# Kernel tuning notes

Measured on AMD Instinct MI355X. Metric: run time of the kernel, lower is better.

Reference implementation:

```python
import jax, jax.numpy as jnp
import numpy as np

T = 65536
OBS_DIM = 64
ACTION_DIM = 16
EMB_DIM = 8  # min(action_dim, 8)
HID = 256
NOBJ = 4
IN_DIM = OBS_DIM + EMB_DIM


def setup_inputs() -> dict:
    key = jax.random.key(0)
    ks = jax.random.split(key, 16)
    g = lambda k, shape, s=0.05: (jax.random.normal(k, shape, dtype=jnp.float32) * s)
    inp = {
        "observations": jax.random.normal(ks[0], (T, OBS_DIM), dtype=jnp.float32),
        "actions": jax.random.randint(ks[1], (T,), 0, ACTION_DIM),
        "emb": g(ks[2], (ACTION_DIM, EMB_DIM)),
        # layer 0 (input_dim -> hidden)
        "Win0": g(ks[3], (HID, IN_DIM)),
        "WB0": g(ks[4], (HID, IN_DIM)),
        "WC0": g(ks[5], (HID, IN_DIM)),
        "Wd0": g(ks[6], (HID, IN_DIM)),
        "Alog0": jax.random.normal(ks[7], (HID,), dtype=jnp.float32),
        # layer 1 (hidden -> hidden)
        "Win1": g(ks[8], (HID, HID)),
        "WB1": g(ks[9], (HID, HID)),
        "WC1": g(ks[10], (HID, HID)),
        "Wd1": g(ks[11], (HID, HID)),
        "Alog1": jax.random.normal(ks[12], (HID,), dtype=jnp.float32),
        # output head
        "Wout": g(ks[13], (NOBJ, HID)),
        "bout": jnp.zeros((NOBJ,), dtype=jnp.float32),
    }
    return inp


def _ssm_layer(x, Win, WB, WC, Wd, Alog):
    """One selective-SSM layer: h_t = exp(delta_t * A) * h_{t-1} + B_t * x_state_t; y = C * h."""
    x_state = x @ Win.T            # [T, H]
    B = x @ WB.T                   # [T, H]
    C = x @ WC.T                   # [T, H]
    delta = jax.nn.sigmoid(x @ Wd.T)  # [T, H]
    A = -jnp.exp(Alog)             # [H]
    A_bar = jnp.exp(delta * A)     # [T, H], decay factors
    Bx = B * x_state               # [T, H], inputs to the recurrence

    def step(h, inputs):
        a, bx = inputs
        h = a * h + bx
        return h, h

    h0 = jnp.zeros((x_state.shape[-1],), dtype=x_state.dtype)
    _, h_seq = jax.lax.scan(step, h0, (A_bar, Bx))
    return C * h_seq


def reference(observations, actions, emb,
              Win0, WB0, WC0, Wd0, Alog0,
              Win1, WB1, WC1, Wd1, Alog1,
              Wout, bout):
    x = jnp.concatenate([observations, emb[actions]], axis=-1)  # [T, IN_DIM]
    x = _ssm_layer(x, Win0, WB0, WC0, Wd0, Alog0)
    x = _ssm_layer(x, Win1, WB1, WC1, Wd1, Alog1)
    out = x @ Wout.T + bout                                     # [T, NOBJ]
    return jax.nn.softplus(out) + 1.0
```

## Files before the change

kernel.cpp:

```cpp
#include <hip/hip_runtime.h>

typedef unsigned short u16;
typedef __attribute__((ext_vector_type(8))) short bf16x8;
typedef __attribute__((ext_vector_type(4))) float f32x4;
typedef __attribute__((ext_vector_type(8))) unsigned short u16x8;

#define T_LEN 65536
#define HID 256
#define K0 96
#define K1 256
#define BM 128
#define BN 128
#define CHUNK 64
#define NCHUNK 1024
#define NSEG 32
#define CPS 32

__device__ __forceinline__ float bf2f(u16 u) {
  unsigned x = ((unsigned)u) << 16; float f; __builtin_memcpy(&f, &x, 4); return f;
}
__device__ __forceinline__ u16 f2bf(float f) {
  unsigned x; __builtin_memcpy(&x, &f, 4);
  x += 0x7FFFu + ((x >> 16) & 1u);
  return (u16)(x >> 16);
}

__device__ __forceinline__ void gl_lds16(const void* g, void* l) {
  __builtin_amdgcn_global_load_lds((const __attribute__((address_space(1))) unsigned int*)g,
                                   (__attribute__((address_space(3))) unsigned int*)l,
                                   16, 0, 0);
}

__global__ __launch_bounds__(256) void build_x0(
    const float* __restrict__ obs, const int* __restrict__ act,
    const float* __restrict__ emb, u16* __restrict__ x0)
{
  const int idx = blockIdx.x * 256 + threadIdx.x;
  const int t = idx / 24, seg = idx - t * 24;
  u16 v0 = 0, v1 = 0, v2 = 0, v3 = 0;
  if (seg < 16) {
    const float4 f = *(const float4*)&obs[(size_t)t * 64 + seg * 4];
    v0 = f2bf(f.x); v1 = f2bf(f.y); v2 = f2bf(f.z); v3 = f2bf(f.w);
  } else if (seg < 18) {
    const int a = act[t];
    const int e0 = (seg - 16) * 4;
    v0 = f2bf(emb[a * 8 + e0 + 0]); v1 = f2bf(emb[a * 8 + e0 + 1]);
    v2 = f2bf(emb[a * 8 + e0 + 2]); v3 = f2bf(emb[a * 8 + e0 + 3]);
  }
  u16* p = &x0[(size_t)t * 96 + seg * 4];
  p[0] = v0; p[1] = v1; p[2] = v2; p[3] = v3;
}

__global__ __launch_bounds__(256) void prep_w(
    const float* __restrict__ Win0, const float* __restrict__ WB0,
    const float* __restrict__ WC0,  const float* __restrict__ Wd0,
    const float* __restrict__ Alog0,
    const float* __restrict__ Win1, const float* __restrict__ WB1,
    const float* __restrict__ WC1,  const float* __restrict__ Wd1,
    const float* __restrict__ Alog1,
    u16* __restrict__ W0v, u16* __restrict__ W1v, float* __restrict__ Aneg)
{
  const int idx = blockIdx.x * 256 + threadIdx.x;
  if (idx < 1024 * K0) {
    const int row = idx / K0, k = idx - row * K0;
    const int h = row >> 2, p = row & 3;
    const float* W = (p == 0) ? Win0 : (p == 1) ? WB0 : (p == 2) ? WC0 : Wd0;
    W0v[idx] = f2bf((k < 72) ? W[h * 72 + k] : 0.f);
  } else if (idx < 1024 * K0 + 1024 * K1) {
    const int j = idx - 1024 * K0;
    const int row = j >> 8, k = j & 255;
    const int h = row >> 2, p = row & 3;
    const float* W = (p == 0) ? Win1 : (p == 1) ? WB1 : (p == 2) ? WC1 : Wd1;
    W1v[j] = f2bf(W[h * 256 + k]);
  } else if (idx < 1024 * K0 + 1024 * K1 + 512) {
    const int j = idx - (1024 * K0 + 1024 * K1);
    Aneg[j] = -__expf((j < 256) ? Alog0[j] : Alog1[j - 256]);
  }
}

template <int KDIM>
__global__ __launch_bounds__(256, 3) void gemm_scan(
    const u16* __restrict__ X, const u16* __restrict__ Wv,
    const float* __restrict__ Aneg,
    u16* __restrict__ hlocb, u16* __restrict__ apfxb, u16* __restrict__ cb,
    float* __restrict__ aprod, float* __restrict__ hlast)
{
  static_assert(KDIM % 32 == 0, "K must be multiple of 32");
  __shared__ u16 sA[BM * 32];
  __shared__ u16 sB[BN * 32];
  __shared__ float sT[64 * 132];
  __shared__ float sAgg[8 * 32 * 2];

  const int tid = threadIdx.x;
  const int l   = tid & 63;
  const int w   = tid >> 6;
  const int n0  = blockIdx.x * BN;
  const int m0  = blockIdx.y * BM;
  const int wm  = (w >> 1) * 64;
  const int wn  = (w & 1) * 64;

  f32x4 acc[4][4];
  const f32x4 zero = {0.f, 0.f, 0.f, 0.f};
#pragma unroll
  for (int mi = 0; mi < 4; ++mi)
#pragma unroll
    for (int ni = 0; ni < 4; ++ni) acc[mi][ni] = zero;

  const int rr = w * 32 + (l >> 2);
  const int kb = (l & 3) * 16;

  for (int ks = 0; ks < KDIM / 32; ++ks) {
    __syncthreads();
#pragma unroll
    for (int i = 0; i < 2; ++i) {
      const char* gA = (const char*)(X + (size_t)(m0 + rr + i * 16) * KDIM + ks * 32) + kb;
      gl_lds16(gA, (char*)sA + w * 2048 + i * 1024);
      const char* gB = (const char*)(Wv + (size_t)(n0 + rr + i * 16) * KDIM + ks * 32) + kb;
      gl_lds16(gB, (char*)sB + w * 2048 + i * 1024);
    }
    __syncthreads();

    bf16x8 af[4], bfr[4];
#pragma unroll
    for (int mi = 0; mi < 4; ++mi)
      af[mi] = *(const bf16x8*)&sA[(wm + mi * 16 + (l & 15)) * 32 + (l >> 4) * 8];
#pragma unroll
    for (int ni = 0; ni < 4; ++ni)
      bfr[ni] = *(const bf16x8*)&sB[(wn + ni * 16 + (l & 15)) * 32 + (l >> 4) * 8];
#pragma unroll
    for (int mi = 0; mi < 4; ++mi)
#pragma unroll
      for (int ni = 0; ni < 4; ++ni)
        acc[mi][ni] = __builtin_amdgcn_mfma_f32_16x16x32_bf16(af[mi], bfr[ni], acc[mi][ni], 0, 0, 0);
  }

  const int q  = tid >> 5;
  const int c  = tid & 31;
  const int ch = (n0 >> 2) + c;
  const float An = Aneg[ch];

  for (int hh = 0; hh < 2; ++hh) {
    __syncthreads();
    if ((w >> 1) == hh) {
#pragma unroll
      for (int mi = 0; mi < 4; ++mi)
#pragma unroll
        for (int ni = 0; ni < 4; ++ni)
#pragma unroll
          for (int v = 0; v < 4; ++v)
            sT[(mi * 16 + (l >> 4) * 4 + v) * 132 + wn + ni * 16 + (l & 15)] = acc[mi][ni][v];
    }
    __syncthreads();

    float Pl[8], Hl[8];
    float ap = 1.f, hl = 0.f;
#pragma unroll
    for (int j = 0; j < 8; ++j) {
      const int tl = q * 8 + j;
      const float pin = sT[tl * 132 + 4 * c + 0];
      const float pB  = sT[tl * 132 + 4 * c + 1];
      const float pC  = sT[tl * 132 + 4 * c + 2];
      const float pd  = sT[tl * 132 + 4 * c + 3];
      const float delta = 1.f / (1.f + __expf(-pd));
      const float a  = __expf(delta * An);
      hl = a * hl + pB * pin;
      ap *= a;
      Pl[j] = ap; Hl[j] = hl;
      cb[(size_t)(m0 + hh * 64 + tl) * HID + ch] = f2bf(pC);
    }
    sAgg[(q * 32 + c) * 2 + 0] = ap;
    sAgg[(q * 32 + c) * 2 + 1] = hl;
    __syncthreads();

    float sap = 1.f, shl = 0.f;
    for (int qq = 0; qq < q; ++qq) {
      const float a_ = sAgg[(qq * 32 + c) * 2 + 0];
      const float h_ = sAgg[(qq * 32 + c) * 2 + 1];
      shl = a_ * shl + h_;
      sap *= a_;
    }
#pragma unroll
    for (int j = 0; j < 8; ++j) {
      const int tl = q * 8 + j;
      const size_t r = (size_t)(m0 + hh * 64 + tl) * HID + ch;
      hlocb[r] = f2bf(Hl[j] + Pl[j] * shl);
      apfxb[r] = f2bf(Pl[j] * sap);
    }
    if (q == 7) {
      const int chunk = blockIdx.y * 2 + hh;
      aprod[(size_t)chunk * HID + ch] = sap * ap;
      hlast[(size_t)chunk * HID + ch] = Hl[7] + Pl[7] * shl;
    }
  }
}

__global__ __launch_bounds__(256) void pass2a(
    const float* __restrict__ aprod, const float* __restrict__ hlast,
    float* __restrict__ clocal, float* __restrict__ apfxc,
    float* __restrict__ segAP, float* __restrict__ segHL)
{
  const int s = blockIdx.x;
  const int h = threadIdx.x;
  float H = 0.f, P = 1.f;
#pragma unroll 4
  for (int j = 0; j < CPS; ++j) {
    const size_t o = (size_t)(s * CPS + j) * HID + h;
    clocal[o] = H; apfxc[o] = P;
    const float a = aprod[o], hh = hlast[o];
    H = a * H + hh;
    P *= a;
  }
  segAP[s * HID + h] = P;
  segHL[s * HID + h] = H;
}

__global__ __launch_bounds__(256) void pass2b(
    const float* __restrict__ segAP, const float* __restrict__ segHL,
    float* __restrict__ segc)
{
  const int h = threadIdx.x;
  float S = 0.f;
#pragma unroll 4
  for (int s = 0; s < NSEG; ++s) {
    segc[s * HID + h] = S;
    S = segAP[s * HID + h] * S + segHL[s * HID + h];
  }
}

__global__ __launch_bounds__(256) void pass2c(
    const float* __restrict__ clocal, const float* __restrict__ apfxc,
    const float* __restrict__ segc, float* __restrict__ carry)
{
  const int ck = blockIdx.x;
  const int h  = threadIdx.x;
  const size_t o = (size_t)ck * HID + h;
  carry[o] = clocal[o] + apfxc[o] * segc[(ck / CPS) * HID + h];
}

__global__ __launch_bounds__(256) void combine(
    const u16* __restrict__ hlocb, const u16* __restrict__ apfxb,
    const u16* __restrict__ cb, const float* __restrict__ carry,
    u16* __restrict__ y)
{
  const size_t v = (size_t)blockIdx.x * 256 + threadIdx.x;
  const int t   = (int)(v >> 5);
  const int ch0 = ((int)v & 31) * 8;
  const u16x8 hl8 = *(const u16x8*)&hlocb[v * 8];
  const u16x8 ap8 = *(const u16x8*)&apfxb[v * 8];
  const u16x8 c8  = *(const u16x8*)&cb[v * 8];
  const float* cr = &carry[(size_t)(t >> 6) * HID + ch0];
  const float4 cr0 = *(const float4*)&cr[0];
  const float4 cr1 = *(const float4*)&cr[4];
  const float crv[8] = {cr0.x, cr0.y, cr0.z, cr0.w, cr1.x, cr1.y, cr1.z, cr1.w};
  u16x8 o;
#pragma unroll
  for (int j = 0; j < 8; ++j)
    o[j] = f2bf(bf2f((u16)c8[j]) * (bf2f((u16)hl8[j]) + bf2f((u16)ap8[j]) * crv[j]));
  *(u16x8*)&y[v * 8] = o;
}

__global__ __launch_bounds__(256) void head(
    const u16* __restrict__ y1, const float* __restrict__ Wout,
    const float* __restrict__ bout, float* __restrict__ out)
{
  __shared__ u16 ly[64 * 264];
  __shared__ float lw[4 * HID];
  __shared__ float lb[4];
  const int tid = threadIdx.x;
  for (int i = tid; i < 4 * HID; i += 256) lw[i] = Wout[i];
  if (tid < 4) lb[tid] = bout[tid];
  const size_t rbase = (size_t)blockIdx.x * 64 * HID;
#pragma unroll
  for (int i = 0; i < 8; ++i) {
    const int lin = i * 256 + tid;
    const int r = lin >> 5, c8 = lin & 31;
    *(u16x8*)&ly[r * 264 + c8 * 8] = *(const u16x8*)&y1[rbase + (size_t)r * HID + c8 * 8];
  }
  __syncthreads();
  const int t = tid >> 2, o = tid & 3;
  float acc = lb[o];
#pragma unroll 8
  for (int h = 0; h < HID; ++h)
    acc += bf2f(ly[t * 264 + h]) * lw[o * HID + h];
  out[((size_t)blockIdx.x * 64 + t) * 4 + o] = logf(1.f + __expf(acc)) + 1.f;
}

extern "C" void kernel_launch(void* const* d_in, const int* in_sizes, int n_in,
                              void* d_out, int out_size, void* d_ws, size_t ws_size,
                              hipStream_t stream)
{
  (void)in_sizes; (void)n_in; (void)out_size; (void)ws_size;
  const float* obs   = (const float*)d_in[0];
  const int*   act   = (const int*)d_in[1];
  const float* emb   = (const float*)d_in[2];
  const float* Win0  = (const float*)d_in[3];
  const float* WB0   = (const float*)d_in[4];
  const float* WC0   = (const float*)d_in[5];
  const float* Wd0   = (const float*)d_in[6];
  const float* Alog0 = (const float*)d_in[7];
  const float* Win1  = (const float*)d_in[8];
  const float* WB1   = (const float*)d_in[9];
  const float* WC1   = (const float*)d_in[10];
  const float* Wd1   = (const float*)d_in[11];
  const float* Alog1 = (const float*)d_in[12];
  const float* Wout  = (const float*)d_in[13];
  const float* bout  = (const float*)d_in[14];
  float* out = (float*)d_out;

  char* ws = (char*)d_ws;
  size_t off = 0;
  auto alloc = [&](size_t bytes) {
    char* p = ws + off;
    off += (bytes + 255) & ~(size_t)255;
    return p;
  };
  u16*   x0    = (u16*)  alloc((size_t)T_LEN * K0 * 2);
  u16*   W0v   = (u16*)  alloc((size_t)1024 * K0 * 2);
  u16*   W1v   = (u16*)  alloc((size_t)1024 * K1 * 2);
  float* Aneg  = (float*)alloc(512 * 4);
  u16*   hlocb = (u16*)  alloc((size_t)T_LEN * HID * 2);
  u16*   apfxb = (u16*)  alloc((size_t)T_LEN * HID * 2);
  u16*   cb    = (u16*)  alloc((size_t)T_LEN * HID * 2);
  u16*   y     = (u16*)  alloc((size_t)T_LEN * HID * 2);
  float* aprod = (float*)alloc((size_t)NCHUNK * HID * 4);
  float* hlast = (float*)alloc((size_t)NCHUNK * HID * 4);
  float* carry = (float*)alloc((size_t)NCHUNK * HID * 4);
  float* clocal= (float*)alloc((size_t)NCHUNK * HID * 4);
  float* apfxc = (float*)alloc((size_t)NCHUNK * HID * 4);
  float* segAP = (float*)alloc((size_t)NSEG * HID * 4);
  float* segHL = (float*)alloc((size_t)NSEG * HID * 4);
  float* segc  = (float*)alloc((size_t)NSEG * HID * 4);

  build_x0<<<T_LEN * 24 / 256, 256, 0, stream>>>(obs, act, emb, x0);
  prep_w<<<(1024 * K0 + 1024 * K1 + 512 + 255) / 256, 256, 0, stream>>>(
      Win0, WB0, WC0, Wd0, Alog0, Win1, WB1, WC1, Wd1, Alog1, W0v, W1v, Aneg);

  gemm_scan<K0><<<dim3(8, T_LEN / BM), 256, 0, stream>>>(x0, W0v, Aneg,
      hlocb, apfxb, cb, aprod, hlast);
  pass2a<<<NSEG, 256, 0, stream>>>(aprod, hlast, clocal, apfxc, segAP, segHL);
  pass2b<<<1, 256, 0, stream>>>(segAP, segHL, segc);
  pass2c<<<NCHUNK, 256, 0, stream>>>(clocal, apfxc, segc, carry);
  combine<<<T_LEN * HID / 8 / 256, 256, 0, stream>>>(hlocb, apfxb, cb, carry, y);

  gemm_scan<K1><<<dim3(8, T_LEN / BM), 256, 0, stream>>>(y, W1v, Aneg + 256,
      hlocb, apfxb, cb, aprod, hlast);
  pass2a<<<NSEG, 256, 0, stream>>>(aprod, hlast, clocal, apfxc, segAP, segHL);
  pass2b<<<1, 256, 0, stream>>>(segAP, segHL, segc);
  pass2c<<<NCHUNK, 256, 0, stream>>>(clocal, apfxc, segc, carry);
  combine<<<T_LEN * HID / 8 / 256, 256, 0, stream>>>(hlocb, apfxb, cb, carry, y);

  head<<<T_LEN / 64, 256, 0, stream>>>(y, Wout, bout, out);
}
```

Before: 294.3 us.

## Premultiply C into packed bf16 pair, fuse carry into combine, XCD-aware tile mapping

The scan kernel now multiplies C into the local state and the prefix product and stores both as one packed 32-bit bf16 pair, instead of three separate bf16 arrays. This cuts intermediate traffic from 6 to 4 bytes per element on both write and read. The pass2c kernel is removed and its carry computation is folded into combine. Blocks are remapped to a 1D grid so each XCD handles a contiguous range of row tiles, which aims to improve L2 locality. Rounding C*h to bf16 before adding the carry term changes numerics slightly.

```diff
diff --git a/kernel.cpp b/kernel.cpp
--- a/kernel.cpp
+++ b/kernel.cpp
@@ -82,7 +82,7 @@
 __global__ __launch_bounds__(256, 3) void gemm_scan(
     const u16* __restrict__ X, const u16* __restrict__ Wv,
     const float* __restrict__ Aneg,
-    u16* __restrict__ hlocb, u16* __restrict__ apfxb, u16* __restrict__ cb,
+    unsigned* __restrict__ uvb,
     float* __restrict__ aprod, float* __restrict__ hlast)
 {
   static_assert(KDIM % 32 == 0, "K must be multiple of 32");
@@ -94,8 +94,13 @@
   const int tid = threadIdx.x;
   const int l   = tid & 63;
   const int w   = tid >> 6;
-  const int n0  = blockIdx.x * BN;
-  const int m0  = blockIdx.y * BM;
+  const int bid = blockIdx.x;
+  const int xcd = bid & 7;
+  const int k_  = bid >> 3;
+  const int mt  = xcd * 64 + (k_ >> 3);
+  const int nt  = k_ & 7;
+  const int m0  = mt * BM;
+  const int n0  = nt * BN;
   const int wm  = (w >> 1) * 64;
   const int wn  = (w & 1) * 64;
 
@@ -152,7 +157,7 @@
     }
     __syncthreads();
 
-    float Pl[8], Hl[8];
+    float Pl[8], Hl[8], Cl[8];
     float ap = 1.f, hl = 0.f;
 #pragma unroll
     for (int j = 0; j < 8; ++j) {
@@ -165,8 +170,7 @@
       const float a  = __expf(delta * An);
       hl = a * hl + pB * pin;
       ap *= a;
-      Pl[j] = ap; Hl[j] = hl;
-      cb[(size_t)(m0 + hh * 64 + tl) * HID + ch] = f2bf(pC);
+      Pl[j] = ap; Hl[j] = hl; Cl[j] = pC;
     }
     sAgg[(q * 32 + c) * 2 + 0] = ap;
     sAgg[(q * 32 + c) * 2 + 1] = hl;
@@ -182,12 +186,14 @@
 #pragma unroll
     for (int j = 0; j < 8; ++j) {
       const int tl = q * 8 + j;
-      const size_t r = (size_t)(m0 + hh * 64 + tl) * HID + ch;
-      hlocb[r] = f2bf(Hl[j] + Pl[j] * shl);
-      apfxb[r] = f2bf(Pl[j] * sap);
+      const float hloc = Hl[j] + Pl[j] * shl;
+      const float vpfx = Pl[j] * sap;
+      const unsigned pack = (unsigned)f2bf(Cl[j] * hloc)
+                          | ((unsigned)f2bf(Cl[j] * vpfx) << 16);
+      uvb[(size_t)(m0 + hh * 64 + tl) * HID + ch] = pack;
     }
     if (q == 7) {
-      const int chunk = blockIdx.y * 2 + hh;
+      const int chunk = mt * 2 + hh;
       aprod[(size_t)chunk * HID + ch] = sap * ap;
       hlast[(size_t)chunk * HID + ch] = Hl[7] + Pl[7] * shl;
     }
@@ -227,36 +233,35 @@
   }
 }
 
-__global__ __launch_bounds__(256) void pass2c(
+__global__ __launch_bounds__(256) void combine(
+    const unsigned* __restrict__ uvb,
     const float* __restrict__ clocal, const float* __restrict__ apfxc,
-    const float* __restrict__ segc, float* __restrict__ carry)
-{
-  const int ck = blockIdx.x;
-  const int h  = threadIdx.x;
-  const size_t o = (size_t)ck * HID + h;
-  carry[o] = clocal[o] + apfxc[o] * segc[(ck / CPS) * HID + h];
-}
-
-__global__ __launch_bounds__(256) void combine(
-    const u16* __restrict__ hlocb, const u16* __restrict__ apfxb,
-    const u16* __restrict__ cb, const float* __restrict__ carry,
-    u16* __restrict__ y)
-{
-  const size_t v = (size_t)blockIdx.x * 256 + threadIdx.x;
-  const int t   = (int)(v >> 5);
-  const int ch0 = ((int)v & 31) * 8;
-  const u16x8 hl8 = *(const u16x8*)&hlocb[v * 8];
-  const u16x8 ap8 = *(const u16x8*)&apfxb[v * 8];
-  const u16x8 c8  = *(const u16x8*)&cb[v * 8];
-  const float* cr = &carry[(size_t)(t >> 6) * HID + ch0];
-  const float4 cr0 = *(const float4*)&cr[0];
-  const float4 cr1 = *(const float4*)&cr[4];
-  const float crv[8] = {cr0.x, cr0.y, cr0.z, cr0.w, cr1.x, cr1.y, cr1.z, cr1.w};
+    const float* __restrict__ segc, u16* __restrict__ y)
+{
+  const size_t vi = (size_t)blockIdx.x * 256 + threadIdx.x;
+  const int t   = (int)(vi >> 5);
+  const int ch0 = ((int)vi & 31) * 8;
+  const int ck  = t >> 6;
+  const int sg  = ck / CPS;
+  const float* cl = &clocal[(size_t)ck * HID + ch0];
+  const float* ax = &apfxc[(size_t)ck * HID + ch0];
+  const float* sc = &segc[(size_t)sg * HID + ch0];
+  const float4 cl0 = *(const float4*)&cl[0], cl1 = *(const float4*)&cl[4];
+  const float4 ax0 = *(const float4*)&ax[0], ax1 = *(const float4*)&ax[4];
+  const float4 sc0 = *(const float4*)&sc[0], sc1 = *(const float4*)&sc[4];
+  const float crv[8] = {
+    cl0.x + ax0.x * sc0.x, cl0.y + ax0.y * sc0.y,
+    cl0.z + ax0.z * sc0.z, cl0.w + ax0.w * sc0.w,
+    cl1.x + ax1.x * sc1.x, cl1.y + ax1.y * sc1.y,
+    cl1.z + ax1.z * sc1.z, cl1.w + ax1.w * sc1.w };
+  const uint4 p0 = *(const uint4*)&uvb[vi * 8];
+  const uint4 p1 = *(const uint4*)&uvb[vi * 8 + 4];
+  const unsigned pk[8] = {p0.x, p0.y, p0.z, p0.w, p1.x, p1.y, p1.z, p1.w};
   u16x8 o;
 #pragma unroll
   for (int j = 0; j < 8; ++j)
-    o[j] = f2bf(bf2f((u16)c8[j]) * (bf2f((u16)hl8[j]) + bf2f((u16)ap8[j]) * crv[j]));
-  *(u16x8*)&y[v * 8] = o;
+    o[j] = f2bf(bf2f((u16)(pk[j] & 0xffffu)) + bf2f((u16)(pk[j] >> 16)) * crv[j]);
+  *(u16x8*)&y[vi * 8] = o;
 }
 
 __global__ __launch_bounds__(256) void head(
@@ -314,40 +319,33 @@
     off += (bytes + 255) & ~(size_t)255;
     return p;
   };
-  u16*   x0    = (u16*)  alloc((size_t)T_LEN * K0 * 2);
-  u16*   W0v   = (u16*)  alloc((size_t)1024 * K0 * 2);
-  u16*   W1v   = (u16*)  alloc((size_t)1024 * K1 * 2);
-  float* Aneg  = (float*)alloc(512 * 4);
-  u16*   hlocb = (u16*)  alloc((size_t)T_LEN * HID * 2);
-  u16*   apfxb = (u16*)  alloc((size_t)T_LEN * HID * 2);
-  u16*   cb    = (u16*)  alloc((size_t)T_LEN * HID * 2);
-  u16*   y     = (u16*)  alloc((size_t)T_LEN * HID * 2);
-  float* aprod = (float*)alloc((size_t)NCHUNK * HID * 4);
-  float* hlast = (float*)alloc((size_t)NCHUNK * HID * 4);
-  float* carry = (float*)alloc((size_t)NCHUNK * HID * 4);
-  float* clocal= (float*)alloc((size_t)NCHUNK * HID * 4);
-  float* apfxc = (float*)alloc((size_t)NCHUNK * HID * 4);
-  float* segAP = (float*)alloc((size_t)NSEG * HID * 4);
-  float* segHL = (float*)alloc((size_t)NSEG * HID * 4);
-  float* segc  = (float*)alloc((size_t)NSEG * HID * 4);
+  u16*      x0    = (u16*)     alloc((size_t)T_LEN * K0 * 2);
+  u16*      W0v   = (u16*)     alloc((size_t)1024 * K0 * 2);
+  u16*      W1v   = (u16*)     alloc((size_t)1024 * K1 * 2);
+  float*    Aneg  = (float*)   alloc(512 * 4);
+  unsigned* uvb   = (unsigned*)alloc((size_t)T_LEN * HID * 4);
+  u16*      y     = (u16*)     alloc((size_t)T_LEN * HID * 2);
+  float*    aprod = (float*)   alloc((size_t)NCHUNK * HID * 4);
+  float*    hlast = (float*)   alloc((size_t)NCHUNK * HID * 4);
+  float*    clocal= (float*)   alloc((size_t)NCHUNK * HID * 4);
+  float*    apfxc = (float*)   alloc((size_t)NCHUNK * HID * 4);
+  float*    segAP = (float*)   alloc((size_t)NSEG * HID * 4);
+  float*    segHL = (float*)   alloc((size_t)NSEG * HID * 4);
+  float*    segc  = (float*)   alloc((size_t)NSEG * HID * 4);
 
   build_x0<<<T_LEN * 24 / 256, 256, 0, stream>>>(obs, act, emb, x0);
   prep_w<<<(1024 * K0 + 1024 * K1 + 512 + 255) / 256, 256, 0, stream>>>(
       Win0, WB0, WC0, Wd0, Alog0, Win1, WB1, WC1, Wd1, Alog1, W0v, W1v, Aneg);
 
-  gemm_scan<K0><<<dim3(8, T_LEN / BM), 256, 0, stream>>>(x0, W0v, Aneg,
-      hlocb, apfxb, cb, aprod, hlast);
+  gemm_scan<K0><<<4096, 256, 0, stream>>>(x0, W0v, Aneg, uvb, aprod, hlast);
   pass2a<<<NSEG, 256, 0, stream>>>(aprod, hlast, clocal, apfxc, segAP, segHL);
   pass2b<<<1, 256, 0, stream>>>(segAP, segHL, segc);
-  pass2c<<<NCHUNK, 256, 0, stream>>>(clocal, apfxc, segc, carry);
-  combine<<<T_LEN * HID / 8 / 256, 256, 0, stream>>>(hlocb, apfxb, cb, carry, y);
-
-  gemm_scan<K1><<<dim3(8, T_LEN / BM), 256, 0, stream>>>(y, W1v, Aneg + 256,
-      hlocb, apfxb, cb, aprod, hlast);
+  combine<<<T_LEN * HID / 8 / 256, 256, 0, stream>>>(uvb, clocal, apfxc, segc, y);
+
+  gemm_scan<K1><<<4096, 256, 0, stream>>>(y, W1v, Aneg + 256, uvb, aprod, hlast);
   pass2a<<<NSEG, 256, 0, stream>>>(aprod, hlast, clocal, apfxc, segAP, segHL);
   pass2b<<<1, 256, 0, stream>>>(segAP, segHL, segc);
-  pass2c<<<NCHUNK, 256, 0, stream>>>(clocal, apfxc, segc, carry);
-  combine<<<T_LEN * HID / 8 / 256, 256, 0, stream>>>(hlocb, apfxb, cb, carry, y);
+  combine<<<T_LEN * HID / 8 / 256, 256, 0, stream>>>(uvb, clocal, apfxc, segc, y);
 
   head<<<T_LEN / 64, 256, 0, stream>>>(y, Wout, bout, out);
 }
```

Measured after the change: 261.0 us. 1.13x faster.
